# Kernel tuning notes

Hardware: AMD Instinct MI355X
Metric: run time of the kernel (lower is better)

Reference implementation:

```python
import jax, jax.numpy as jnp
import numpy as np

B, L, D_MODEL, HEAD = 8, 2048, 1024, 64

def setup_inputs() -> dict:
    key = jax.random.key(0)
    ks = jax.random.split(key, 6)
    idx_k = jax.random.normal(ks[0], (B, L, D_MODEL), dtype=jnp.float32)
    idx_q = jax.random.normal(ks[1], (B, L, D_MODEL), dtype=jnp.float32)
    idx_v = jax.random.normal(ks[2], (B, L, D_MODEL), dtype=jnp.float32)
    # causal lower-triangular mask, broadcast over batch
    msk = jnp.tril(jnp.ones((L, L), dtype=jnp.int32))
    s = 1.0 / np.sqrt(D_MODEL)
    Wk = jax.random.uniform(ks[3], (D_MODEL, HEAD), jnp.float32, -s, s)
    Wq = jax.random.uniform(ks[4], (D_MODEL, HEAD), jnp.float32, -s, s)
    Wv = jax.random.uniform(ks[5], (D_MODEL, HEAD), jnp.float32, -s, s)
    return {"idx_k": idx_k, "idx_q": idx_q, "idx_v": idx_v, "msk": msk,
            "Wk": Wk, "Wq": Wq, "Wv": Wv}

def reference(idx_k, idx_q, idx_v, msk, Wk, Wq, Wv):
    # projections (Linear, no bias): [B,L,d_model] @ [d_model,head] -> [B,L,head]
    K = idx_k @ Wk
    Q = idx_q @ Wq
    V = idx_v @ Wv
    scale = K.shape[-1] ** -0.5
    # scores: [B,Lq,Lk]
    S = jnp.einsum('bqh,bkh->bqk', Q, K) * scale
    S = jnp.where(msk == 0, jnp.float32(-1e9), S)
    att = jax.nn.softmax(S, axis=-1)  # dropout=0.0 (inference)
    out = jnp.einsum('bqk,bkh->bqh', att, V)
    return out
```

## Files before the change

### kernel.cpp

```cpp
#include <hip/hip_runtime.h>

typedef __bf16 bf16x8 __attribute__((ext_vector_type(8)));
typedef float f32x4 __attribute__((ext_vector_type(4)));
typedef unsigned short u16;

#define LSEQ 2048
#define DMODEL 1024
#define HEADD 64
#define NBATCH 8

__device__ __forceinline__ u16 cvt(float f) {
  __bf16 h = (__bf16)f;
  return __builtin_bit_cast(u16, h);
}

__global__ __launch_bounds__(256) void wt_kernel(
    const float* __restrict__ Wk, const float* __restrict__ Wq,
    const float* __restrict__ Wv, u16* __restrict__ wp) {
  int idx = blockIdx.x * 256 + threadIdx.x;
  int j = idx & 7;
  int lane = (idx >> 3) & 63;
  int ks = (idx >> 9) & 31;
  int c = (idx >> 14) & 3;
  int p = idx >> 16;
  const float* W = (p == 0) ? Wk : ((p == 1) ? Wq : Wv);
  int k = ks * 32 + 8 * (lane >> 4) + j;
  int col = 16 * c + (lane & 15);
  wp[idx] = cvt(W[(size_t)k * HEADD + col]);
}

__global__ __launch_bounds__(256) void proj_kernel(
    const float* __restrict__ ik, const float* __restrict__ iq, const float* __restrict__ iv,
    const u16* __restrict__ wp, u16* __restrict__ Kb, u16* __restrict__ Qb,
    u16* __restrict__ Vt) {
  __shared__ __align__(16) u16 Asw[2][64 * 128];
  int p = blockIdx.y;
  const float* A = (p == 0) ? ik : ((p == 1) ? iq : iv);
  const u16* Wp = wp + (size_t)p * 4 * 32 * 512;
  int t = threadIdx.x;
  int lane = t & 63;
  int wv = t >> 6;
  int l15 = lane & 15, g = lane >> 4;
  int rowbase = blockIdx.x * 64;
  const float* srcbase = A + (size_t)rowbase * DMODEL;

  int srow0 = t >> 5;
  int scol = (t & 31) * 4;

  float4 stg[8];
  auto issue = [&](int kc) {
#pragma unroll
    for (int i = 0; i < 8; ++i) {
      int row = i * 8 + srow0;
      stg[i] = *(const float4*)(srcbase + (size_t)row * DMODEL + kc + scol);
    }
  };
  auto commit = [&](int buf) {
    char* base = (char*)&Asw[buf][0];
#pragma unroll
    for (int i = 0; i < 8; ++i) {
      int row = i * 8 + srow0;
      ushort4 pk;
      pk.x = cvt(stg[i].x); pk.y = cvt(stg[i].y);
      pk.z = cvt(stg[i].z); pk.w = cvt(stg[i].w);
      int byte = row * 256 + ((scol * 2) ^ ((row & 7) << 4));
      *(ushort4*)(base + byte) = pk;
    }
  };

  f32x4 acc[4] = {};
  int arow = 16 * wv + l15;
  int abase = arow * 256;
  int aswz = (l15 & 7) << 4;

  issue(0);
  commit(0);
  __syncthreads();

  for (int c8 = 0; c8 < 8; ++c8) {
    bf16x8 wfr[4][4];
#pragma unroll
    for (int ks = 0; ks < 4; ++ks)
#pragma unroll
      for (int c = 0; c < 4; ++c)
        wfr[ks][c] = *(const bf16x8*)(Wp + ((size_t)c * 32 + c8 * 4 + ks) * 512 + lane * 8);

    __builtin_amdgcn_sched_barrier(0);

    if (c8 < 7) issue((c8 + 1) * 128);

    __builtin_amdgcn_sched_barrier(0);

    const char* lbase = (const char*)&Asw[c8 & 1][0];
#pragma unroll
    for (int ks = 0; ks < 4; ++ks) {
      bf16x8 af = *(const bf16x8*)(lbase + abase + ((ks * 64 + 16 * g) ^ aswz));
#pragma unroll
      for (int c = 0; c < 4; ++c)
        acc[c] = __builtin_amdgcn_mfma_f32_16x16x32_bf16(af, wfr[ks][c], acc[c], 0, 0, 0);
    }

    if (c8 < 7) commit((c8 + 1) & 1);
    __syncthreads();
  }

  int rb2 = rowbase + 16 * wv;
  if (p == 2) {
    int row0 = rb2 + 4 * g;
    int b = row0 >> 11, tok = row0 & 2047;
#pragma unroll
    for (int c = 0; c < 4; ++c) {
      int d = 16 * c + l15;
      ushort4 pk;
      pk.x = cvt(acc[c][0]); pk.y = cvt(acc[c][1]);
      pk.z = cvt(acc[c][2]); pk.w = cvt(acc[c][3]);
      *(ushort4*)(Vt + ((size_t)b * HEADD + d) * LSEQ + tok) = pk;
    }
  } else {
    u16* dst = (p == 0) ? Kb : Qb;
    float s = (p == 1) ? 0.125f : 1.0f;
#pragma unroll
    for (int c = 0; c < 4; ++c)
#pragma unroll
      for (int r = 0; r < 4; ++r)
        dst[(size_t)(rb2 + 4 * g + r) * HEADD + 16 * c + l15] = cvt(acc[c][r] * s);
  }
}

__global__ __launch_bounds__(128) void attn_kernel(
    const u16* __restrict__ Kb, const u16* __restrict__ Qb, const u16* __restrict__ Vt,
    float* __restrict__ out) {
  __shared__ __align__(16) u16 plds[2][16 * 40];
  int lane = threadIdx.x & 63;
  int wv = threadIdx.x >> 6;
  int l15 = lane & 15, g = lane >> 4;
  int b = blockIdx.y;
  int qt = 63 - (int)blockIdx.x;
  int qbase = qt * 32 + wv * 16;

  const u16* Qp = Qb + ((size_t)b * LSEQ + qbase) * HEADD;
  const u16* Kp = Kb + (size_t)b * LSEQ * HEADD;
  const u16* Vp = Vt + (size_t)b * HEADD * LSEQ;

  bf16x8 qf[2];
#pragma unroll
  for (int ds = 0; ds < 2; ++ds)
    qf[ds] = *(const bf16x8*)(Qp + (size_t)l15 * HEADD + 32 * ds + 8 * g);

  f32x4 acc[4] = {};
  float m = -1e30f, lsum = 0.f;
  int q_abs = qbase + l15;
  int ntiles = (qbase + 47) >> 5;

  for (int t = 0; t < ntiles; ++t) {
    int kbase = t * 32;
    f32x4 sacc[2] = {};
#pragma unroll
    for (int f = 0; f < 2; ++f)
#pragma unroll
      for (int ds = 0; ds < 2; ++ds) {
        bf16x8 kf = *(const bf16x8*)(Kp + (size_t)(kbase + 16 * f + l15) * HEADD + 32 * ds + 8 * g);
        sacc[f] = __builtin_amdgcn_mfma_f32_16x16x32_bf16(kf, qf[ds], sacc[f], 0, 0, 0);
      }

    float sv[2][4];
    float tmax = -1e30f;
#pragma unroll
    for (int f = 0; f < 2; ++f)
#pragma unroll
      for (int r = 0; r < 4; ++r) {
        int key = kbase + 16 * f + 4 * g + r;
        float s = (key <= q_abs) ? sacc[f][r] : -1e30f;
        sv[f][r] = s;
        tmax = fmaxf(tmax, s);
      }
    tmax = fmaxf(tmax, __shfl_xor(tmax, 16));
    tmax = fmaxf(tmax, __shfl_xor(tmax, 32));
    float mnew = fmaxf(m, tmax);
    float al = __expf(m - mnew);
    float pv[2][4];
    float rs = 0.f;
#pragma unroll
    for (int f = 0; f < 2; ++f)
#pragma unroll
      for (int r = 0; r < 4; ++r) {
        pv[f][r] = __expf(sv[f][r] - mnew);
        rs += pv[f][r];
      }
    rs += __shfl_xor(rs, 16);
    rs += __shfl_xor(rs, 32);
    lsum = lsum * al + rs;
    m = mnew;

    float alr[4];
#pragma unroll
    for (int r = 0; r < 4; ++r) alr[r] = __shfl(al, 4 * g + r);
#pragma unroll
    for (int c = 0; c < 4; ++c)
#pragma unroll
      for (int r = 0; r < 4; ++r) acc[c][r] *= alr[r];

#pragma unroll
    for (int f = 0; f < 2; ++f) {
      ushort4 pk;
      pk.x = cvt(pv[f][0]); pk.y = cvt(pv[f][1]);
      pk.z = cvt(pv[f][2]); pk.w = cvt(pv[f][3]);
      *(ushort4*)&plds[wv][l15 * 40 + 16 * f + 4 * g] = pk;
    }
    bf16x8 ap = *(const bf16x8*)&plds[wv][l15 * 40 + 8 * g];

#pragma unroll
    for (int c = 0; c < 4; ++c) {
      bf16x8 vf = *(const bf16x8*)(Vp + (size_t)(16 * c + l15) * LSEQ + kbase + 8 * g);
      acc[c] = __builtin_amdgcn_mfma_f32_16x16x32_bf16(ap, vf, acc[c], 0, 0, 0);
    }
  }

  float li[4];
#pragma unroll
  for (int r = 0; r < 4; ++r) {
    float lv = __shfl(lsum, 4 * g + r);
    li[r] = 1.0f / lv;
  }
#pragma unroll
  for (int c = 0; c < 4; ++c)
#pragma unroll
    for (int r = 0; r < 4; ++r)
      out[((size_t)b * LSEQ + qbase + 4 * g + r) * HEADD + 16 * c + l15] = acc[c][r] * li[r];
}

extern "C" void kernel_launch(void* const* d_in, const int* in_sizes, int n_in,
                              void* d_out, int out_size, void* d_ws, size_t ws_size,
                              hipStream_t stream) {
  const float* idx_k = (const float*)d_in[0];
  const float* idx_q = (const float*)d_in[1];
  const float* idx_v = (const float*)d_in[2];
  const float* Wk = (const float*)d_in[4];
  const float* Wq = (const float*)d_in[5];
  const float* Wv = (const float*)d_in[6];
  float* out = (float*)d_out;

  char* ws = (char*)d_ws;
  const size_t WT_BYTES = (size_t)3 * 4 * 32 * 512 * 2;
  const size_t MAT_BYTES = (size_t)NBATCH * LSEQ * HEADD * 2;
  u16* wp = (u16*)ws;
  u16* Kb = (u16*)(ws + WT_BYTES);
  u16* Qb = (u16*)(ws + WT_BYTES + MAT_BYTES);
  u16* Vt = (u16*)(ws + WT_BYTES + 2 * MAT_BYTES);

  hipLaunchKernelGGL(wt_kernel, dim3(768), dim3(256), 0, stream, Wk, Wq, Wv, wp);
  hipLaunchKernelGGL(proj_kernel, dim3(256, 3), dim3(256), 0, stream,
                     idx_k, idx_q, idx_v, wp, Kb, Qb, Vt);
  hipLaunchKernelGGL(attn_kernel, dim3(64, NBATCH), dim3(128), 0, stream, Kb, Qb, Vt, out);
}
```

Baseline: 101.2 us.

## Split attention keys across waves with merge; double-stage projection register prefetch

```diff
diff --git a/kernel.cpp b/kernel.cpp
--- a/kernel.cpp
+++ b/kernel.cpp
@@ -13,6 +13,13 @@
   __bf16 h = (__bf16)f;
   return __builtin_bit_cast(u16, h);
 }
+
+#define BARRIER_LGKM() do {                                   \
+    asm volatile("s_waitcnt lgkmcnt(0)" ::: "memory");        \
+    __builtin_amdgcn_sched_barrier(0);                        \
+    __builtin_amdgcn_s_barrier();                             \
+    __builtin_amdgcn_sched_barrier(0);                        \
+  } while (0)
 
 __global__ __launch_bounds__(256) void wt_kernel(
     const float* __restrict__ Wk, const float* __restrict__ Wq,
@@ -47,16 +54,16 @@
   int srow0 = t >> 5;
   int scol = (t & 31) * 4;
 
-  float4 stg[8];
-  auto issue = [&](int kc) {
-#pragma unroll
-    for (int i = 0; i < 8; ++i) {
-      int row = i * 8 + srow0;
-      stg[i] = *(const float4*)(srcbase + (size_t)row * DMODEL + kc + scol);
-    }
-  };
-  auto commit = [&](int buf) {
-    char* base = (char*)&Asw[buf][0];
+  float4 stgA[8], stgB[8];
+  bf16x8 wfr[4][4];
+
+  auto issue = [&](float4 (&stg)[8], int kc) {
+#pragma unroll
+    for (int i = 0; i < 8; ++i)
+      stg[i] = *(const float4*)(srcbase + (size_t)(i * 8 + srow0) * DMODEL + kc + scol);
+  };
+  auto commit = [&](const float4 (&stg)[8], u16* basep) {
+    char* base = (char*)basep;
 #pragma unroll
     for (int i = 0; i < 8; ++i) {
       int row = i * 8 + srow0;
@@ -67,31 +74,19 @@
       *(ushort4*)(base + byte) = pk;
     }
   };
-
-  f32x4 acc[4] = {};
-  int arow = 16 * wv + l15;
-  int abase = arow * 256;
-  int aswz = (l15 & 7) << 4;
-
-  issue(0);
-  commit(0);
-  __syncthreads();
-
-  for (int c8 = 0; c8 < 8; ++c8) {
-    bf16x8 wfr[4][4];
+  auto wload = [&](int c8) {
 #pragma unroll
     for (int ks = 0; ks < 4; ++ks)
 #pragma unroll
       for (int c = 0; c < 4; ++c)
         wfr[ks][c] = *(const bf16x8*)(Wp + ((size_t)c * 32 + c8 * 4 + ks) * 512 + lane * 8);
-
-    __builtin_amdgcn_sched_barrier(0);
-
-    if (c8 < 7) issue((c8 + 1) * 128);
-
-    __builtin_amdgcn_sched_barrier(0);
-
-    const char* lbase = (const char*)&Asw[c8 & 1][0];
+  };
+
+  f32x4 acc[4] = {};
+  int abase = (16 * wv + l15) * 256;
+  int aswz = (l15 & 7) << 4;
+
+  auto computeC = [&](const char* lbase) {
 #pragma unroll
     for (int ks = 0; ks < 4; ++ks) {
       bf16x8 af = *(const bf16x8*)(lbase + abase + ((ks * 64 + 16 * g) ^ aswz));
@@ -99,9 +94,29 @@
       for (int c = 0; c < 4; ++c)
         acc[c] = __builtin_amdgcn_mfma_f32_16x16x32_bf16(af, wfr[ks][c], acc[c], 0, 0, 0);
     }
-
-    if (c8 < 7) commit((c8 + 1) & 1);
-    __syncthreads();
+  };
+
+  issue(stgA, 0);
+  issue(stgB, 128);
+  commit(stgA, &Asw[0][0]);
+  BARRIER_LGKM();
+
+#pragma unroll 1
+  for (int cc = 0; cc < 8; cc += 2) {
+    wload(cc);
+    __builtin_amdgcn_sched_barrier(0);
+    if (cc < 6) issue(stgA, (cc + 2) * 128);
+    __builtin_amdgcn_sched_barrier(0);
+    computeC((const char*)&Asw[0][0]);
+    commit(stgB, &Asw[1][0]);
+    BARRIER_LGKM();
+    wload(cc + 1);
+    __builtin_amdgcn_sched_barrier(0);
+    if (cc < 5) issue(stgB, (cc + 3) * 128);
+    __builtin_amdgcn_sched_barrier(0);
+    computeC((const char*)&Asw[1][0]);
+    if (cc < 6) commit(stgA, &Asw[0][0]);
+    BARRIER_LGKM();
   }
 
   int rb2 = rowbase + 16 * wv;
@@ -131,12 +146,13 @@
     const u16* __restrict__ Kb, const u16* __restrict__ Qb, const u16* __restrict__ Vt,
     float* __restrict__ out) {
   __shared__ __align__(16) u16 plds[2][16 * 40];
+  __shared__ __align__(16) float mrg[64][18];
   int lane = threadIdx.x & 63;
   int wv = threadIdx.x >> 6;
   int l15 = lane & 15, g = lane >> 4;
   int b = blockIdx.y;
-  int qt = 63 - (int)blockIdx.x;
-  int qbase = qt * 32 + wv * 16;
+  int qt = 127 - (int)blockIdx.x;
+  int qbase = qt * 16;
 
   const u16* Qp = Qb + ((size_t)b * LSEQ + qbase) * HEADD;
   const u16* Kp = Kb + (size_t)b * LSEQ * HEADD;
@@ -152,7 +168,7 @@
   int q_abs = qbase + l15;
   int ntiles = (qbase + 47) >> 5;
 
-  for (int t = 0; t < ntiles; ++t) {
+  for (int t = wv; t < ntiles; t += 2) {
     int kbase = t * 32;
     f32x4 sacc[2] = {};
 #pragma unroll
@@ -216,17 +232,35 @@
     }
   }
 
-  float li[4];
-#pragma unroll
-  for (int r = 0; r < 4; ++r) {
-    float lv = __shfl(lsum, 4 * g + r);
-    li[r] = 1.0f / lv;
-  }
-#pragma unroll
-  for (int c = 0; c < 4; ++c)
-#pragma unroll
-    for (int r = 0; r < 4; ++r)
-      out[((size_t)b * LSEQ + qbase + 4 * g + r) * HEADD + 16 * c + l15] = acc[c][r] * li[r];
+  if (wv == 1) {
+#pragma unroll
+    for (int c = 0; c < 4; ++c)
+#pragma unroll
+      for (int r = 0; r < 4; ++r) mrg[lane][c * 4 + r] = acc[c][r];
+    mrg[lane][16] = m;
+    mrg[lane][17] = lsum;
+  }
+  __syncthreads();
+  if (wv == 0) {
+    float m1 = mrg[lane][16], l1 = mrg[lane][17];
+    float mT = fmaxf(m, m1);
+    float e0 = __expf(m - mT), e1 = __expf(m1 - mT);
+    float lT = lsum * e0 + l1 * e1;
+    float e0r[4], e1r[4], li[4];
+#pragma unroll
+    for (int r = 0; r < 4; ++r) {
+      e0r[r] = __shfl(e0, 4 * g + r);
+      e1r[r] = __shfl(e1, 4 * g + r);
+      li[r] = 1.0f / __shfl(lT, 4 * g + r);
+    }
+#pragma unroll
+    for (int c = 0; c < 4; ++c)
+#pragma unroll
+      for (int r = 0; r < 4; ++r) {
+        float v = acc[c][r] * e0r[r] + mrg[lane][c * 4 + r] * e1r[r];
+        out[((size_t)b * LSEQ + qbase + 4 * g + r) * HEADD + 16 * c + l15] = v * li[r];
+      }
+  }
 }
 
 extern "C" void kernel_launch(void* const* d_in, const int* in_sizes, int n_in,
@@ -251,5 +285,5 @@
   hipLaunchKernelGGL(wt_kernel, dim3(768), dim3(256), 0, stream, Wk, Wq, Wv, wp);
   hipLaunchKernelGGL(proj_kernel, dim3(256, 3), dim3(256), 0, stream,
                      idx_k, idx_q, idx_v, wp, Kb, Qb, Vt);
-  hipLaunchKernelGGL(attn_kernel, dim3(64, NBATCH), dim3(128), 0, stream, Kb, Qb, Vt, out);
-}
+  hipLaunchKernelGGL(attn_kernel, dim3(128, NBATCH), dim3(128), 0, stream, Kb, Qb, Vt, out);
+}
```

After: 102.9 us. No clear change (+1.7%).
